# Performance work log

Hardware: AMD Instinct MI355X
Metric: run time of the kernel (lower is better)

Reference implementation:

```python
import jax, jax.numpy as jnp
import numpy as np

D = 512       # d_model
H = 8         # n_heads
HD = D // H   # head_dim = 64
BS = 64       # block_size
B = 1
S = 8192
NB = S // BS  # 128 blocks
THRESH = 0.3


def setup_inputs() -> dict:
    key = jax.random.key(0)
    ks = jax.random.split(key, 6)
    sc = 0.02
    return {
        "x": jax.random.normal(ks[0], (B, S, D), jnp.float32),
        "w_qkv": (jax.random.normal(ks[1], (D, 3 * D)) * sc).astype(jnp.float32),
        "b_qkv": jnp.zeros((3 * D,), jnp.float32),
        "w_out": (jax.random.normal(ks[2], (D, D)) * sc).astype(jnp.float32),
        "b_out": jnp.zeros((D,), jnp.float32),
        "w_r1": (jax.random.normal(ks[3], (D, 128)) * sc).astype(jnp.float32),
        "b_r1": jnp.zeros((128,), jnp.float32),
        "w_r2": (jax.random.normal(ks[4], (128, 1)) * sc).astype(jnp.float32),
        "b_r2": jnp.full((1,), 0.5, jnp.float32),  # sigmoid(~0.5)>0.3 -> non-degenerate mask
    }


def reference(x, w_qkv, b_qkv, w_out, b_out, w_r1, b_r1, w_r2, b_r2):
    Bx, Sx, Dx = x.shape
    qkv = (x @ w_qkv + b_qkv).reshape(Bx, Sx, 3, H, HD)
    q = jnp.transpose(qkv[:, :, 0], (0, 2, 1, 3))  # [B,H,S,HD]
    k = jnp.transpose(qkv[:, :, 1], (0, 2, 1, 3))
    v = jnp.transpose(qkv[:, :, 2], (0, 2, 1, 3))

    # --- router: per-block importance from mean-pooled q block (d_model features) ---
    qb = q.reshape(Bx, H, NB, BS, HD)
    rep = jnp.transpose(qb.mean(axis=3), (0, 2, 1, 3)).reshape(Bx, NB, Dx)  # [B,NB,D]
    imp = jax.nn.sigmoid(jax.nn.relu(rep @ w_r1 + b_r1) @ w_r2 + b_r2)[..., 0]  # [B,NB]
    keep = (imp.mean(axis=0) >= THRESH).astype(x.dtype)  # [NB], shared across batch (torch uses batch-mean)

    kb = k.reshape(Bx, H, NB, BS, HD)
    vb = v.reshape(Bx, H, NB, BS, HD)
    tri = jnp.triu(jnp.ones((BS, BS), bool), 1)  # strict upper triangle within diagonal block
    jidx = jnp.arange(NB)
    scale = 1.0 / np.sqrt(HD)

    def step(carry, i):
        q_i = jax.lax.dynamic_slice_in_dim(q, i * BS, BS, axis=2)        # [B,H,BSq,HD]
        s = jnp.einsum('bhqd,bhjkd->bhqjk', q_i, kb) * scale             # [B,H,BSq,NB,BSk]
        causal = (jidx == i)[None, :, None] & tri[:, None, :]            # [BSq,NB,BSk]
        s = jnp.where(causal[None, None], -jnp.inf, s)
        p = jax.nn.softmax(s, axis=-1)                                   # softmax PER key-block (as in torch loop)
        wj = keep * keep[i]                                              # block pair gate [NB]
        o = jnp.einsum('bhqjk,j,bhjkd->bhqd', p, wj, vb)                 # sum of gated per-block contributions
        return carry, o

    _, outs = jax.lax.scan(step, None, jnp.arange(NB))                   # [NB,B,H,BSq,HD]
    attn = jnp.transpose(outs, (1, 2, 0, 3, 4)).reshape(Bx, H, Sx, HD)
    attn = jnp.transpose(attn, (0, 2, 1, 3)).reshape(Bx, Sx, Dx)
    return attn @ w_out + b_out
```

## Files before the change

### kernel.cpp

```cpp
#include <hip/hip_runtime.h>

typedef unsigned short u16;
typedef unsigned int u32;
typedef __attribute__((ext_vector_type(8))) short short8;
typedef __attribute__((ext_vector_type(4))) short short4v;
typedef __attribute__((ext_vector_type(4))) float f32x4;
typedef __attribute__((ext_vector_type(4))) float float4v;
typedef __attribute__((ext_vector_type(2))) u32 u32x2;
typedef __attribute__((ext_vector_type(4))) u32 u32x4;

#define S_LEN 8192
#define NHEAD 8
#define NBLK  128
#define SCALE_C 0.18033688011112042f

__device__ __forceinline__ u16 f2b(float f) {
    union { float f; unsigned u; } v; v.f = f;
    unsigned r = v.u + 0x7FFFu + ((v.u >> 16) & 1u);
    return (u16)(r >> 16);
}
__device__ __forceinline__ float b2f(u16 b) {
    union { float f; unsigned u; } v; v.u = ((unsigned)b) << 16; return v.f;
}
__device__ __forceinline__ u32 cvt_pk_bf16(float lo, float hi) {
    u32 r;
    asm("v_cvt_pk_bf16_f32 %0, %1, %2" : "=v"(r) : "v"(lo), "v"(hi));
    return r;
}
__device__ __forceinline__ void pl16swap(u32& a, u32& b) {
    u32x2 r = __builtin_amdgcn_permlane16_swap(a, b, false, false);
    a = r[0]; b = r[1];
}
__device__ __forceinline__ void pl32swap(u32& a, u32& b) {
    u32x2 r = __builtin_amdgcn_permlane32_swap(a, b, false, false);
    a = r[0]; b = r[1];
}
__device__ __forceinline__ int swz(int row, int colByte) {
    return row * 128 + (colByte ^ ((row & 7) << 4));
}
__device__ __forceinline__ void gload_lds(const void* g, void* l) {
    __builtin_amdgcn_global_load_lds(
        (const __attribute__((address_space(1))) void*)g,
        (__attribute__((address_space(3))) void*)l, 16, 0, 0);
}

__global__ __launch_bounds__(256) void cvt_x_kernel(const float* __restrict__ x, u16* __restrict__ xb) {
    int idx = blockIdx.x * 256 + threadIdx.x;
    float4v v = *((const float4v*)x + idx);
    short4v o;
    #pragma unroll
    for (int r = 0; r < 4; ++r) o[r] = (short)f2b(v[r]);
    *((short4v*)xb + idx) = o;
}

__global__ __launch_bounds__(256) void cvt_T_kernel(const float* __restrict__ w, u16* __restrict__ wt, int C) {
    int idx = blockIdx.x * 256 + threadIdx.x;
    int r = idx & 511, cc = idx >> 9;
    wt[idx] = f2b(w[(size_t)r * C + cc]);
}

__device__ __forceinline__ void gemm128_core(const u16* __restrict__ A,
                                             const u16* __restrict__ Bt,
                                             int m0, int n0, char* As, char* Bs,
                                             f32x4 acc[4][4]) {
    const int tid = threadIdx.x;
    const int lane = tid & 63, wid = tid >> 6;
    const int q16 = lane >> 4, l16 = lane & 15;
    const int wm = wid >> 1, wn = wid & 1;
    #pragma unroll 1
    for (int kt = 0; kt < 8; ++kt) {
        const int k0 = kt * 64;
        __syncthreads();
        #pragma unroll
        for (int p = 0; p < 4; ++p) {
            int c = tid + p * 256;
            int row = c >> 3, colp = (c & 7) ^ (row & 7);
            char* dst = (char*)0 + (wid * 64 + p * 256) * 16;
            gload_lds(A  + (size_t)(m0 + row) * 512 + k0 + colp * 8, As + (size_t)(wid * 64 + p * 256) * 16);
            gload_lds(Bt + (size_t)(n0 + row) * 512 + k0 + colp * 8, Bs + (size_t)(wid * 64 + p * 256) * 16);
            (void)dst;
        }
        __syncthreads();
        #pragma unroll
        for (int kk = 0; kk < 2; ++kk) {
            short8 a[4], b[4];
            #pragma unroll
            for (int t = 0; t < 4; ++t) {
                int arow = wm * 64 + t * 16 + l16;
                a[t] = *(const short8*)(As + swz(arow, kk * 64 + q16 * 16));
                int brow = wn * 64 + t * 16 + l16;
                b[t] = *(const short8*)(Bs + swz(brow, kk * 64 + q16 * 16));
            }
            #pragma unroll
            for (int mt = 0; mt < 4; ++mt)
                #pragma unroll
                for (int nt = 0; nt < 4; ++nt)
                    acc[mt][nt] = __builtin_amdgcn_mfma_f32_16x16x32_bf16(a[mt], b[nt], acc[mt][nt], 0, 0, 0);
        }
    }
}

__global__ __launch_bounds__(256) void qkv_gemm(const u16* __restrict__ xb, const u16* __restrict__ wqkvT,
                                                const float* __restrict__ bqkv,
                                                u16* __restrict__ qb, u16* __restrict__ kb, u16* __restrict__ vt) {
    __shared__ char smem[32768];
    f32x4 acc[4][4];
    #pragma unroll
    for (int a = 0; a < 4; ++a)
        #pragma unroll
        for (int b = 0; b < 4; ++b) acc[a][b] = (f32x4){0.f, 0.f, 0.f, 0.f};
    const int m0 = blockIdx.x * 128, n0 = blockIdx.y * 128;
    gemm128_core(xb, wqkvT, m0, n0, smem, smem + 16384, acc);

    const int lane = threadIdx.x & 63, wid = threadIdx.x >> 6;
    const int q16 = lane >> 4, l16 = lane & 15;
    const int wm = wid >> 1, wn = wid & 1;
    #pragma unroll
    for (int mt = 0; mt < 4; ++mt) {
        #pragma unroll
        for (int nt = 0; nt < 4; ++nt) {
            int n = n0 + wn * 64 + nt * 16 + l16;
            float bias = bqkv[n];
            int t = n >> 9, h = (n >> 6) & 7, d = n & 63;
            int sb = m0 + wm * 64 + mt * 16 + q16 * 4;
            f32x4 v = acc[mt][nt];
            if (t == 2) {
                short4v pk;
                #pragma unroll
                for (int r = 0; r < 4; ++r) pk[r] = (short)f2b(v[r] + bias);
                *(short4v*)(vt + (size_t)(h * 64 + d) * S_LEN + sb) = pk;
            } else {
                u16* dst = (t == 0) ? qb : kb;
                float scale = (t == 0) ? SCALE_C : 1.0f;
                #pragma unroll
                for (int r = 0; r < 4; ++r)
                    dst[(size_t)(h * S_LEN + sb + r) * 64 + d] = f2b((v[r] + bias) * scale);
            }
        }
    }
}

__global__ __launch_bounds__(256) void out_gemm(const u16* __restrict__ a0, const u16* __restrict__ a1,
                                                const u16* __restrict__ wotT,
                                                const float* __restrict__ bout, float* __restrict__ out) {
    __shared__ char smem[32768];
    f32x4 acc[4][4];
    #pragma unroll
    for (int a = 0; a < 4; ++a)
        #pragma unroll
        for (int b = 0; b < 4; ++b) acc[a][b] = (f32x4){0.f, 0.f, 0.f, 0.f};
    const int m0 = blockIdx.x * 128, n0 = blockIdx.y * 128;
    gemm128_core(a0, wotT, m0, n0, smem, smem + 16384, acc);
    gemm128_core(a1, wotT, m0, n0, smem, smem + 16384, acc);

    const int lane = threadIdx.x & 63, wid = threadIdx.x >> 6;
    const int q16 = lane >> 4, l16 = lane & 15;
    const int wm = wid >> 1, wn = wid & 1;
    #pragma unroll
    for (int mt = 0; mt < 4; ++mt) {
        #pragma unroll
        for (int nt = 0; nt < 4; ++nt) {
            int n = n0 + wn * 64 + nt * 16 + l16;
            float bias = bout[n];
            int sb = m0 + wm * 64 + mt * 16 + q16 * 4;
            #pragma unroll
            for (int r = 0; r < 4; ++r)
                out[(size_t)(sb + r) * 512 + n] = acc[mt][nt][r] + bias;
        }
    }
}

__global__ __launch_bounds__(256) void router_kernel(const u16* __restrict__ qb,
                                                     const float* __restrict__ w_r1, const float* __restrict__ b_r1,
                                                     const float* __restrict__ w_r2, const float* __restrict__ b_r2,
                                                     float* __restrict__ keepf) {
    const int nb = blockIdx.x, tid = threadIdx.x;
    __shared__ float rep[512];
    __shared__ float h1[128];
    for (int dim = tid; dim < 512; dim += 256) {
        int h = dim >> 6, d = dim & 63;
        const u16* p = qb + (size_t)(h * S_LEN + nb * 64) * 64 + d;
        float s = 0.f;
        #pragma unroll 4
        for (int t = 0; t < 64; ++t) s += b2f(p[t * 64]);
        rep[dim] = s * (0.015625f / SCALE_C);
    }
    __syncthreads();
    if (tid < 128) {
        float a = b_r1[tid];
        for (int k = 0; k < 512; ++k) a += rep[k] * w_r1[k * 128 + tid];
        h1[tid] = fmaxf(a, 0.f);
    }
    __syncthreads();
    if (tid < 64) {
        float v = h1[tid] * w_r2[tid] + h1[tid + 64] * w_r2[tid + 64];
        #pragma unroll
        for (int off = 32; off; off >>= 1) v += __shfl_down(v, off);
        if (tid == 0) {
            float z = v + b_r2[0];
            keepf[nb] = (z >= -0.84729786f) ? 1.0f : 0.0f;
        }
    }
}

__global__ __launch_bounds__(256, 4) void attn_kernel(const u16* __restrict__ qb, const u16* __restrict__ kb,
                                                      const u16* __restrict__ vt, const float* __restrict__ keepf,
                                                      u16* __restrict__ att0, u16* __restrict__ att1) {
    const int i = blockIdx.x, h = blockIdx.y, jh = blockIdx.z;
    const int j0 = jh * 64;
    u16* __restrict__ att = jh ? att1 : att0;
    const int tid = threadIdx.x, lane = tid & 63, wid = tid >> 6;
    const int q16 = lane >> 4, l16 = lane & 15;
    __shared__ char smem[32768];

    short8 bq[2][2];
    #pragma unroll
    for (int qh = 0; qh < 2; ++qh) {
        const u16* qrow = qb + (size_t)(h * S_LEN + i * 128 + wid * 32 + qh * 16 + l16) * 64;
        bq[qh][0] = *(const short8*)(qrow + q16 * 8);
        bq[qh][1] = *(const short8*)(qrow + 32 + q16 * 8);
    }
    const int kq = i * 2 + (wid >> 1);
    const float keep_i = keepf[kq];
    const int qloc = (wid & 1) * 32 + l16;

    f32x4 o[2][4];
    #pragma unroll
    for (int qh = 0; qh < 2; ++qh)
        #pragma unroll
        for (int t = 0; t < 4; ++t) o[qh][t] = (f32x4){0.f, 0.f, 0.f, 0.f};

    const int rA = tid >> 3,          cA = (tid & 7) ^ (rA & 7);
    const int rB = (tid + 256) >> 3,  cB = (tid & 7) ^ (rB & 7);
    const u16* kb_h = kb + (size_t)h * S_LEN * 64;
    const u16* vt_h = vt + (size_t)h * 64 * S_LEN;
    const int ldw0 = wid * 1024, ldw1 = wid * 1024 + 4096;

    {
        char* base = smem;
        gload_lds(kb_h + (size_t)(j0 * 64 + rA) * 64 + cA * 8, base + ldw0);
        gload_lds(kb_h + (size_t)(j0 * 64 + rB) * 64 + cB * 8, base + ldw1);
        gload_lds(vt_h + (size_t)rA * S_LEN + j0 * 64 + cA * 8, base + 8192 + ldw0);
        gload_lds(vt_h + (size_t)rB * S_LEN + j0 * 64 + cB * 8, base + 8192 + ldw1);
    }
    __syncthreads();

    for (int jj = 0; jj < 64; ++jj) {
        const int j = j0 + jj;
        char* Kc = smem + ((jj & 1) << 14);
        char* Vc = Kc + 8192;
        if (jj < 63) {
            char* Kn = smem + (((jj + 1) & 1) << 14);
            gload_lds(kb_h + (size_t)((j + 1) * 64 + rA) * 64 + cA * 8, Kn + ldw0);
            gload_lds(kb_h + (size_t)((j + 1) * 64 + rB) * 64 + cB * 8, Kn + ldw1);
            gload_lds(vt_h + (size_t)rA * S_LEN + (j + 1) * 64 + cA * 8, Kn + 8192 + ldw0);
            gload_lds(vt_h + (size_t)rB * S_LEN + (j + 1) * 64 + cB * 8, Kn + 8192 + ldw1);
        }
        const float gj = keep_i * keepf[j];

        f32x4 s4[2][4];
        __builtin_amdgcn_s_setprio(1);
        #pragma unroll
        for (int n0 = 0; n0 < 4; ++n0) {
            short8 ka0 = *(const short8*)(Kc + swz(n0 * 16 + l16, q16 * 16));
            short8 ka1 = *(const short8*)(Kc + swz(n0 * 16 + l16, 64 + q16 * 16));
            #pragma unroll
            for (int qh = 0; qh < 2; ++qh) {
                f32x4 a = (f32x4){0.f, 0.f, 0.f, 0.f};
                a = __builtin_amdgcn_mfma_f32_16x16x32_bf16(ka0, bq[qh][0], a, 0, 0, 0);
                a = __builtin_amdgcn_mfma_f32_16x16x32_bf16(ka1, bq[qh][1], a, 0, 0, 0);
                s4[qh][n0] = a;
            }
        }
        __builtin_amdgcn_s_setprio(0);

        short8 pb[2][2];
        #pragma unroll
        for (int qh = 0; qh < 2; ++qh) {
            float pv[4][4];
            #pragma unroll
            for (int n0 = 0; n0 < 4; ++n0)
                #pragma unroll
                for (int r = 0; r < 4; ++r)
                    pv[n0][r] = __builtin_amdgcn_exp2f(s4[qh][n0][r]);
            if (j == kq) {
                const int qthis = qloc + qh * 16;
                #pragma unroll
                for (int n0 = 0; n0 < 4; ++n0)
                    #pragma unroll
                    for (int r = 0; r < 4; ++r)
                        if (n0 * 16 + q16 * 4 + r > qthis) pv[n0][r] = 0.f;
            }
            float sum = 0.f;
            #pragma unroll
            for (int n0 = 0; n0 < 4; ++n0)
                sum += (pv[n0][0] + pv[n0][1]) + (pv[n0][2] + pv[n0][3]);
            {
                u32 sa = __builtin_bit_cast(u32, sum), sb = sa;
                pl16swap(sa, sb);
                sum = __builtin_bit_cast(float, sa) + __builtin_bit_cast(float, sb);
                u32 sc = __builtin_bit_cast(u32, sum), sd = sc;
                pl32swap(sc, sd);
                sum = __builtin_bit_cast(float, sc) + __builtin_bit_cast(float, sd);
            }
            const float rinv = gj * __builtin_amdgcn_rcpf(sum);
            u32 dw[4][2];
            #pragma unroll
            for (int n0 = 0; n0 < 4; ++n0) {
                dw[n0][0] = cvt_pk_bf16(pv[n0][0] * rinv, pv[n0][1] * rinv);
                dw[n0][1] = cvt_pk_bf16(pv[n0][2] * rinv, pv[n0][3] * rinv);
            }
            #pragma unroll
            for (int kk = 0; kk < 2; ++kk) {
                u32 a0 = dw[2 * kk][0], b0 = dw[2 * kk + 1][0];
                pl32swap(a0, b0);
                pl16swap(a0, b0);
                u32 a1 = dw[2 * kk][1], b1 = dw[2 * kk + 1][1];
                pl32swap(a1, b1);
                pl16swap(a1, b1);
                u32x4 wv;
                wv[0] = a0; wv[1] = a1; wv[2] = b0; wv[3] = b1;
                pb[qh][kk] = __builtin_bit_cast(short8, wv);
            }
        }

        __builtin_amdgcn_s_setprio(1);
        #pragma unroll
        for (int dt = 0; dt < 4; ++dt) {
            short8 va0 = *(const short8*)(Vc + swz(dt * 16 + l16, q16 * 16));
            short8 va1 = *(const short8*)(Vc + swz(dt * 16 + l16, 64 + q16 * 16));
            #pragma unroll
            for (int qh = 0; qh < 2; ++qh) {
                o[qh][dt] = __builtin_amdgcn_mfma_f32_16x16x32_bf16(va0, pb[qh][0], o[qh][dt], 0, 0, 0);
                o[qh][dt] = __builtin_amdgcn_mfma_f32_16x16x32_bf16(va1, pb[qh][1], o[qh][dt], 0, 0, 0);
            }
        }
        __builtin_amdgcn_s_setprio(0);

        __syncthreads();
    }

    #pragma unroll
    for (int qh = 0; qh < 2; ++qh) {
        u16* obase = att + (size_t)(i * 128 + wid * 32 + qh * 16 + l16) * 512 + h * 64 + q16 * 4;
        #pragma unroll
        for (int dt = 0; dt < 4; ++dt) {
            u32x2 st;
            st[0] = cvt_pk_bf16(o[qh][dt][0], o[qh][dt][1]);
            st[1] = cvt_pk_bf16(o[qh][dt][2], o[qh][dt][3]);
            *(u32x2*)(obase + dt * 16) = st;
        }
    }
}

static const size_t OFF_XB    = 0;
static const size_t OFF_WQKVT = OFF_XB    + (8u << 20);
static const size_t OFF_WOTT  = OFF_WQKVT + (2u << 20);
static const size_t OFF_QB    = OFF_WOTT  + (1u << 20);
static const size_t OFF_KB    = OFF_QB    + (8u << 20);
static const size_t OFF_VT    = OFF_KB    + (8u << 20);
static const size_t OFF_ATT   = OFF_VT    + (8u << 20);
static const size_t OFF_KEEP  = OFF_ATT   + (8u << 20);

extern "C" void kernel_launch(void* const* d_in, const int* in_sizes, int n_in,
                              void* d_out, int out_size, void* d_ws, size_t ws_size,
                              hipStream_t stream) {
    const float* x     = (const float*)d_in[0];
    const float* w_qkv = (const float*)d_in[1];
    const float* b_qkv = (const float*)d_in[2];
    const float* w_out = (const float*)d_in[3];
    const float* b_out = (const float*)d_in[4];
    const float* w_r1  = (const float*)d_in[5];
    const float* b_r1  = (const float*)d_in[6];
    const float* w_r2  = (const float*)d_in[7];
    const float* b_r2  = (const float*)d_in[8];
    float* out = (float*)d_out;
    char* ws = (char*)d_ws;
    u16* xb     = (u16*)(ws + OFF_XB);
    u16* wqkvT  = (u16*)(ws + OFF_WQKVT);
    u16* wotT   = (u16*)(ws + OFF_WOTT);
    u16* qb     = (u16*)(ws + OFF_QB);
    u16* kb     = (u16*)(ws + OFF_KB);
    u16* vt     = (u16*)(ws + OFF_VT);
    u16* attnb  = (u16*)(ws + OFF_ATT);
    u16* att1   = (u16*)(ws + OFF_XB);
    float* keepf = (float*)(ws + OFF_KEEP);

    cvt_x_kernel<<<4096, 256, 0, stream>>>(x, xb);
    cvt_T_kernel<<<3072, 256, 0, stream>>>(w_qkv, wqkvT, 1536);
    cvt_T_kernel<<<1024, 256, 0, stream>>>(w_out, wotT, 512);
    qkv_gemm<<<dim3(64, 12), 256, 0, stream>>>(xb, wqkvT, b_qkv, qb, kb, vt);
    router_kernel<<<128, 256, 0, stream>>>(qb, w_r1, b_r1, w_r2, b_r2, keepf);
    attn_kernel<<<dim3(64, 8, 2), 256, 0, stream>>>(qb, kb, vt, keepf, attnb, att1);
    out_gemm<<<dim3(64, 4), 256, 0, stream>>>(attnb, att1, wotT, b_out, out);
}
```

Measured before the change: 243.5 us.

## Split attention key range four ways with fp32 atomics and fragment-ordered K/V

The QKV GEMM now writes K and V in a per-block layout that already matches the MFMA fragment order. Attention can then stage tiles with contiguous loads and read LDS without swizzle arithmetic. The key-block range is split into four chunks instead of two, which doubles the grid. Partial outputs are combined through fp32 atomicAdd into a zeroed buffer, then converted to bf16 so the output GEMM runs a single K pass. The gain in parallelism costs a 16MB memset, many global atomics, and an extra conversion kernel.

```diff
diff --git a/kernel.cpp b/kernel.cpp
--- a/kernel.cpp
+++ b/kernel.cpp
@@ -75,10 +75,8 @@
         for (int p = 0; p < 4; ++p) {
             int c = tid + p * 256;
             int row = c >> 3, colp = (c & 7) ^ (row & 7);
-            char* dst = (char*)0 + (wid * 64 + p * 256) * 16;
             gload_lds(A  + (size_t)(m0 + row) * 512 + k0 + colp * 8, As + (size_t)(wid * 64 + p * 256) * 16);
             gload_lds(Bt + (size_t)(n0 + row) * 512 + k0 + colp * 8, Bs + (size_t)(wid * 64 + p * 256) * 16);
-            (void)dst;
         }
         __syncthreads();
         #pragma unroll
@@ -102,7 +100,7 @@
 
 __global__ __launch_bounds__(256) void qkv_gemm(const u16* __restrict__ xb, const u16* __restrict__ wqkvT,
                                                 const float* __restrict__ bqkv,
-                                                u16* __restrict__ qb, u16* __restrict__ kb, u16* __restrict__ vt) {
+                                                u16* __restrict__ qb, u16* __restrict__ kf, u16* __restrict__ vf) {
     __shared__ char smem[32768];
     f32x4 acc[4][4];
     #pragma unroll
@@ -124,24 +122,32 @@
             int t = n >> 9, h = (n >> 6) & 7, d = n & 63;
             int sb = m0 + wm * 64 + mt * 16 + q16 * 4;
             f32x4 v = acc[mt][nt];
-            if (t == 2) {
+            if (t == 0) {
+                #pragma unroll
+                for (int r = 0; r < 4; ++r)
+                    qb[(size_t)(h * S_LEN + sb + r) * 64 + d] = f2b((v[r] + bias) * SCALE_C);
+            } else if (t == 1) {
+                int j = sb >> 6, key = sb & 63;
+                int n0k = key >> 4, c = d >> 5, q16k = (d >> 3) & 3, e = d & 7;
+                int ub = (n0k * 2 + c) * 64 + q16k * 16 + (key & 15);
+                u16* base = kf + (size_t)h * 524288 + (size_t)j * 4096 + e;
+                #pragma unroll
+                for (int r = 0; r < 4; ++r)
+                    base[(ub + r) * 8] = f2b(v[r] + bias);
+            } else {
+                int j = sb >> 6, key = sb & 63;
+                int dt = d >> 4, c = key >> 5, q16v = (key >> 3) & 3, e0 = key & 7;
+                int u = (dt * 2 + c) * 64 + q16v * 16 + (d & 15);
                 short4v pk;
                 #pragma unroll
                 for (int r = 0; r < 4; ++r) pk[r] = (short)f2b(v[r] + bias);
-                *(short4v*)(vt + (size_t)(h * 64 + d) * S_LEN + sb) = pk;
-            } else {
-                u16* dst = (t == 0) ? qb : kb;
-                float scale = (t == 0) ? SCALE_C : 1.0f;
-                #pragma unroll
-                for (int r = 0; r < 4; ++r)
-                    dst[(size_t)(h * S_LEN + sb + r) * 64 + d] = f2b((v[r] + bias) * scale);
-            }
-        }
-    }
-}
-
-__global__ __launch_bounds__(256) void out_gemm(const u16* __restrict__ a0, const u16* __restrict__ a1,
-                                                const u16* __restrict__ wotT,
+                *(short4v*)(vf + (size_t)h * 524288 + (size_t)j * 4096 + u * 8 + e0) = pk;
+            }
+        }
+    }
+}
+
+__global__ __launch_bounds__(256) void out_gemm(const u16* __restrict__ a0, const u16* __restrict__ wotT,
                                                 const float* __restrict__ bout, float* __restrict__ out) {
     __shared__ char smem[32768];
     f32x4 acc[4][4];
@@ -151,7 +157,6 @@
         for (int b = 0; b < 4; ++b) acc[a][b] = (f32x4){0.f, 0.f, 0.f, 0.f};
     const int m0 = blockIdx.x * 128, n0 = blockIdx.y * 128;
     gemm128_core(a0, wotT, m0, n0, smem, smem + 16384, acc);
-    gemm128_core(a1, wotT, m0, n0, smem, smem + 16384, acc);
 
     const int lane = threadIdx.x & 63, wid = threadIdx.x >> 6;
     const int q16 = lane >> 4, l16 = lane & 15;
@@ -203,12 +208,11 @@
     }
 }
 
-__global__ __launch_bounds__(256, 4) void attn_kernel(const u16* __restrict__ qb, const u16* __restrict__ kb,
-                                                      const u16* __restrict__ vt, const float* __restrict__ keepf,
-                                                      u16* __restrict__ att0, u16* __restrict__ att1) {
+__global__ __launch_bounds__(256, 4) void attn_kernel(const u16* __restrict__ qb, const u16* __restrict__ kf,
+                                                      const u16* __restrict__ vf, const float* __restrict__ keepf,
+                                                      float* __restrict__ attF) {
     const int i = blockIdx.x, h = blockIdx.y, jh = blockIdx.z;
-    const int j0 = jh * 64;
-    u16* __restrict__ att = jh ? att1 : att0;
+    const int j0 = jh * 32;
     const int tid = threadIdx.x, lane = tid & 63, wid = tid >> 6;
     const int q16 = lane >> 4, l16 = lane & 15;
     __shared__ char smem[32768];
@@ -230,31 +234,32 @@
         #pragma unroll
         for (int t = 0; t < 4; ++t) o[qh][t] = (f32x4){0.f, 0.f, 0.f, 0.f};
 
-    const int rA = tid >> 3,          cA = (tid & 7) ^ (rA & 7);
-    const int rB = (tid + 256) >> 3,  cB = (tid & 7) ^ (rB & 7);
-    const u16* kb_h = kb + (size_t)h * S_LEN * 64;
-    const u16* vt_h = vt + (size_t)h * 64 * S_LEN;
-    const int ldw0 = wid * 1024, ldw1 = wid * 1024 + 4096;
+    const u16* kf_h = kf + (size_t)h * 524288;
+    const u16* vf_h = vf + (size_t)h * 524288;
+    const int lb = lane * 16;
+    const int stoff = (wid * 128 + lane) * 8;
+    const int ldw = wid * 2048;
 
     {
-        char* base = smem;
-        gload_lds(kb_h + (size_t)(j0 * 64 + rA) * 64 + cA * 8, base + ldw0);
-        gload_lds(kb_h + (size_t)(j0 * 64 + rB) * 64 + cB * 8, base + ldw1);
-        gload_lds(vt_h + (size_t)rA * S_LEN + j0 * 64 + cA * 8, base + 8192 + ldw0);
-        gload_lds(vt_h + (size_t)rB * S_LEN + j0 * 64 + cB * 8, base + 8192 + ldw1);
+        const size_t b = (size_t)j0 * 4096;
+        gload_lds(kf_h + b + stoff,       smem + ldw);
+        gload_lds(kf_h + b + stoff + 512, smem + ldw + 1024);
+        gload_lds(vf_h + b + stoff,       smem + 8192 + ldw);
+        gload_lds(vf_h + b + stoff + 512, smem + 8192 + ldw + 1024);
     }
     __syncthreads();
 
-    for (int jj = 0; jj < 64; ++jj) {
+    for (int jj = 0; jj < 32; ++jj) {
         const int j = j0 + jj;
         char* Kc = smem + ((jj & 1) << 14);
         char* Vc = Kc + 8192;
-        if (jj < 63) {
+        if (jj < 31) {
             char* Kn = smem + (((jj + 1) & 1) << 14);
-            gload_lds(kb_h + (size_t)((j + 1) * 64 + rA) * 64 + cA * 8, Kn + ldw0);
-            gload_lds(kb_h + (size_t)((j + 1) * 64 + rB) * 64 + cB * 8, Kn + ldw1);
-            gload_lds(vt_h + (size_t)rA * S_LEN + (j + 1) * 64 + cA * 8, Kn + 8192 + ldw0);
-            gload_lds(vt_h + (size_t)rB * S_LEN + (j + 1) * 64 + cB * 8, Kn + 8192 + ldw1);
+            const size_t b = (size_t)(j + 1) * 4096;
+            gload_lds(kf_h + b + stoff,       Kn + ldw);
+            gload_lds(kf_h + b + stoff + 512, Kn + ldw + 1024);
+            gload_lds(vf_h + b + stoff,       Kn + 8192 + ldw);
+            gload_lds(vf_h + b + stoff + 512, Kn + 8192 + ldw + 1024);
         }
         const float gj = keep_i * keepf[j];
 
@@ -262,8 +267,8 @@
         __builtin_amdgcn_s_setprio(1);
         #pragma unroll
         for (int n0 = 0; n0 < 4; ++n0) {
-            short8 ka0 = *(const short8*)(Kc + swz(n0 * 16 + l16, q16 * 16));
-            short8 ka1 = *(const short8*)(Kc + swz(n0 * 16 + l16, 64 + q16 * 16));
+            short8 ka0 = *(const short8*)(Kc + n0 * 2048 + lb);
+            short8 ka1 = *(const short8*)(Kc + n0 * 2048 + 1024 + lb);
             #pragma unroll
             for (int qh = 0; qh < 2; ++qh) {
                 f32x4 a = (f32x4){0.f, 0.f, 0.f, 0.f};
@@ -327,8 +332,8 @@
         __builtin_amdgcn_s_setprio(1);
         #pragma unroll
         for (int dt = 0; dt < 4; ++dt) {
-            short8 va0 = *(const short8*)(Vc + swz(dt * 16 + l16, q16 * 16));
-            short8 va1 = *(const short8*)(Vc + swz(dt * 16 + l16, 64 + q16 * 16));
+            short8 va0 = *(const short8*)(Vc + dt * 2048 + lb);
+            short8 va1 = *(const short8*)(Vc + dt * 2048 + 1024 + lb);
             #pragma unroll
             for (int qh = 0; qh < 2; ++qh) {
                 o[qh][dt] = __builtin_amdgcn_mfma_f32_16x16x32_bf16(va0, pb[qh][0], o[qh][dt], 0, 0, 0);
@@ -342,25 +347,23 @@
 
     #pragma unroll
     for (int qh = 0; qh < 2; ++qh) {
-        u16* obase = att + (size_t)(i * 128 + wid * 32 + qh * 16 + l16) * 512 + h * 64 + q16 * 4;
-        #pragma unroll
-        for (int dt = 0; dt < 4; ++dt) {
-            u32x2 st;
-            st[0] = cvt_pk_bf16(o[qh][dt][0], o[qh][dt][1]);
-            st[1] = cvt_pk_bf16(o[qh][dt][2], o[qh][dt][3]);
-            *(u32x2*)(obase + dt * 16) = st;
-        }
-    }
-}
-
-static const size_t OFF_XB    = 0;
-static const size_t OFF_WQKVT = OFF_XB    + (8u << 20);
-static const size_t OFF_WOTT  = OFF_WQKVT + (2u << 20);
-static const size_t OFF_QB    = OFF_WOTT  + (1u << 20);
-static const size_t OFF_KB    = OFF_QB    + (8u << 20);
-static const size_t OFF_VT    = OFF_KB    + (8u << 20);
-static const size_t OFF_ATT   = OFF_VT    + (8u << 20);
-static const size_t OFF_KEEP  = OFF_ATT   + (8u << 20);
+        float* obase = attF + (size_t)(i * 128 + wid * 32 + qh * 16 + l16) * 512 + h * 64 + q16 * 4;
+        #pragma unroll
+        for (int dt = 0; dt < 4; ++dt)
+            #pragma unroll
+            for (int r = 0; r < 4; ++r)
+                atomicAdd(&obase[dt * 16 + r], o[qh][dt][r]);
+    }
+}
+
+static const size_t OFF_WQKVT = 0;
+static const size_t OFF_WOTT  = (size_t)2u << 20;
+static const size_t OFF_QB    = (size_t)3u << 20;
+static const size_t OFF_KB    = (size_t)11u << 20;
+static const size_t OFF_VT    = (size_t)19u << 20;
+static const size_t OFF_ATTF  = (size_t)27u << 20;
+static const size_t OFF_XB    = (size_t)35u << 20;
+static const size_t OFF_KEEP  = (size_t)43u << 20;
 
 extern "C" void kernel_launch(void* const* d_in, const int* in_sizes, int n_in,
                               void* d_out, int out_size, void* d_ws, size_t ws_size,
@@ -376,21 +379,23 @@
     const float* b_r2  = (const float*)d_in[8];
     float* out = (float*)d_out;
     char* ws = (char*)d_ws;
-    u16* xb     = (u16*)(ws + OFF_XB);
     u16* wqkvT  = (u16*)(ws + OFF_WQKVT);
     u16* wotT   = (u16*)(ws + OFF_WOTT);
     u16* qb     = (u16*)(ws + OFF_QB);
-    u16* kb     = (u16*)(ws + OFF_KB);
-    u16* vt     = (u16*)(ws + OFF_VT);
-    u16* attnb  = (u16*)(ws + OFF_ATT);
-    u16* att1   = (u16*)(ws + OFF_XB);
+    u16* kf     = (u16*)(ws + OFF_KB);
+    u16* vf     = (u16*)(ws + OFF_VT);
+    float* attF = (float*)(ws + OFF_ATTF);
+    u16* xb     = (u16*)(ws + OFF_XB);
+    u16* attnb  = (u16*)(ws + OFF_QB);
     float* keepf = (float*)(ws + OFF_KEEP);
 
     cvt_x_kernel<<<4096, 256, 0, stream>>>(x, xb);
     cvt_T_kernel<<<3072, 256, 0, stream>>>(w_qkv, wqkvT, 1536);
     cvt_T_kernel<<<1024, 256, 0, stream>>>(w_out, wotT, 512);
-    qkv_gemm<<<dim3(64, 12), 256, 0, stream>>>(xb, wqkvT, b_qkv, qb, kb, vt);
+    qkv_gemm<<<dim3(64, 12), 256, 0, stream>>>(xb, wqkvT, b_qkv, qb, kf, vf);
     router_kernel<<<128, 256, 0, stream>>>(qb, w_r1, b_r1, w_r2, b_r2, keepf);
-    attn_kernel<<<dim3(64, 8, 2), 256, 0, stream>>>(qb, kb, vt, keepf, attnb, att1);
-    out_gemm<<<dim3(64, 4), 256, 0, stream>>>(attnb, att1, wotT, b_out, out);
-}
+    hipMemsetAsync(ws + OFF_ATTF, 0, (size_t)16u << 20, stream);
+    attn_kernel<<<dim3(64, 8, 4), 256, 0, stream>>>(qb, kf, vf, keepf, attF);
+    cvt_x_kernel<<<4096, 256, 0, stream>>>(attF, attnb);
+    out_gemm<<<dim3(64, 4), 256, 0, stream>>>(attnb, wotT, b_out, out);
+}
```

New measurement: 365.4 us. 50.1% more time.
